# Optimization experiments

Hardware: AMD Instinct MI355X
Metric: run time of the kernel (lower is better)

The kernel has to match this reference:

```python
import jax, jax.numpy as jnp
import numpy as np

G = 7          # grid_size
A = 2          # anchors_per_cell
C = 3          # num_classes
L_COORD, L_OBJ, L_NOOBJ, L_CLS = 5.0, 1.0, 0.5, 2.0


def setup_inputs() -> dict:
    key = jax.random.key(0)
    k0, k1, k2, k3, k4 = jax.random.split(key, 5)
    B, M = 32768, 20
    predictions = jax.random.normal(k0, (B, G, G, A, 5 + C), dtype=jnp.float32)
    xy1 = jax.random.uniform(k1, (B, M, 2), dtype=jnp.float32) * 0.8
    wh = jax.random.uniform(k2, (B, M, 2), dtype=jnp.float32) * 0.19 + 0.01
    target_boxes = jnp.concatenate([xy1, xy1 + wh], axis=-1)  # valid x1<x2, y1<y2
    target_labels = jax.random.randint(k3, (B, M), 0, C, dtype=jnp.int32)
    num_objs = jax.random.randint(k4, (B,), 0, M + 1, dtype=jnp.int32)
    anchors = jnp.array([[0.971, 1.7338], [3.4579, 5.1653]], dtype=jnp.float32)
    class_weights = jnp.array([1.0, 4.9, 4.8], dtype=jnp.float32)
    return dict(predictions=predictions, target_boxes=target_boxes,
                target_labels=target_labels, num_objs=num_objs,
                anchors=anchors, class_weights=class_weights)


def assign_targets(target_boxes, target_labels, num_objs, anchors, B):
    """Vectorized scatter-based replacement of the nested python assignment loop."""
    M = target_boxes.shape[1]
    x1, y1, x2, y2 = [target_boxes[..., i] for i in range(4)]  # (B,M)
    cx, cy = (x1 + x2) * 0.5, (y1 + y2) * 0.5
    w, h = x2 - x1, y2 - y1
    valid = (w > 0) & (h > 0) & (jnp.arange(M)[None, :] < num_objs[:, None])
    gi = jnp.clip(jnp.floor(cy * G).astype(jnp.int32), 0, G - 1)
    gj = jnp.clip(jnp.floor(cx * G).astype(jnp.int32), 0, G - 1)
    wg, hg = w * G, h * G
    # anchor matching IoU (width/height only), (B,M,A)
    inter = jnp.minimum(wg[..., None], anchors[:, 0]) * jnp.minimum(hg[..., None], anchors[:, 1])
    union = (wg * hg)[..., None] + anchors[:, 0] * anchors[:, 1] - inter
    best_a = jnp.argmax(inter / (union + 1e-6), axis=-1).astype(jnp.int32)  # first max = torch loop tie-break
    aw = anchors[best_a, 0]
    ah = anchors[best_a, 1]
    tx = cx * G - gj.astype(jnp.float32)
    ty = cy * G - gi.astype(jnp.float32)
    tw = jnp.log(jnp.clip(wg, 0.01, None) / (aw + 1e-6))
    th = jnp.log(jnp.clip(hg, 0.01, None) / (ah + 1e-6))
    tvals = jnp.stack([tx, ty, tw, th], axis=-1)  # (B,M,4)
    N = B * G * G * A
    bidx = jnp.arange(B, dtype=jnp.int32)[:, None]
    flat = ((bidx * G + gi) * G + gj) * A + best_a  # (B,M)
    flat = jnp.where(valid, flat, N)                # invalid -> dropped by scatter
    idx = flat.ravel()
    obj_mask = jnp.zeros((N,), jnp.float32).at[idx].set(1.0, mode='drop')
    target_bbox = jnp.zeros((N, 4), jnp.float32).at[idx].set(tvals.reshape(-1, 4), mode='drop')
    target_cls = jnp.zeros((N,), jnp.int32).at[idx].set(target_labels.ravel(), mode='drop')
    shape = (B, G, G, A)
    return obj_mask.reshape(shape), target_bbox.reshape(shape + (4,)), target_cls.reshape(shape)


def reference(predictions, target_boxes, target_labels, num_objs, anchors, class_weights):
    B = predictions.shape[0]
    pred_obj = predictions[..., 0]
    pred_bbox = predictions[..., 1:5]
    pred_cls = predictions[..., 5:]
    m, target_bbox, target_cls = assign_targets(target_boxes, target_labels, num_objs, anchors, B)
    sp = jax.nn.softplus
    # BCE-with-logits: target is 1 on obj cells, 0 on noobj cells
    loss_obj = jnp.sum(m * sp(-pred_obj))
    loss_noobj = jnp.sum((1.0 - m) * sp(pred_obj))
    # smooth L1 (beta=1), summed over obj cells
    d = pred_bbox - target_bbox
    ad = jnp.abs(d)
    sl1 = jnp.where(ad < 1.0, 0.5 * d * d, ad - 0.5)
    loss_bbox = jnp.sum(m[..., None] * sl1)
    # weighted cross entropy on obj cells
    logZ = jax.nn.logsumexpimport if False else jax.scipy.special.logsumexp(pred_cls, axis=-1)
    logit_t = jnp.take_along_axis(pred_cls, target_cls[..., None], axis=-1)[..., 0]
    loss_cls = jnp.sum(m * class_weights[target_cls] * (logZ - logit_t))
    num_pos = jnp.maximum(jnp.sum(m), 1.0)
    total = (L_COORD * loss_bbox + L_OBJ * loss_obj + L_NOOBJ * loss_noobj + L_CLS * loss_cls) / num_pos
    return total
```

## Files before the change

### kernel.cpp

```cpp
#include <hip/hip_runtime.h>


namespace {
constexpr int kG = 7;
constexpr int kA = 2;
constexpr int kM = 20;
constexpr int kCells = kG * kG * kA;
constexpr int kCh = 8;
constexpr int kWavesA = 8;
constexpr int kBlockA = 64 * kWavesA;
constexpr int kBlockN = 256;
constexpr int kUnroll = 8;
constexpr int kChunksPerBlk = kBlockN * kUnroll;
}

typedef float f32x4 __attribute__((ext_vector_type(4)));

__device__ __forceinline__ float softplus_fast(float x) {
    return fmaxf(x, 0.0f) + __logf(1.0f + __expf(-fabsf(x)));
}

__global__ __launch_bounds__(kBlockA) void det_loss_assign(
    const float* __restrict__ preds,
    const float4* __restrict__ tboxes4,
    const int* __restrict__ tlabels,
    const int* __restrict__ nobjs,
    const float* __restrict__ anchors,
    const float* __restrict__ cweights,
    float* __restrict__ partialA,
    int B, int NA)
{
    __shared__ float s_red[kWavesA][5];

    const int tid  = threadIdx.x;
    const int wave = tid >> 6;
    const int m    = tid & 63;
    const int wb   = blockIdx.x * kWavesA + wave;
    const bool active = (wb < B);

    const float a00 = anchors[0], a01 = anchors[1];
    const float a10 = anchors[2], a11 = anchors[3];

    int nob = 0;
    if (active && m == 0) nob = nobjs[wb];
    nob = __shfl(nob, 0, 64);

    int cell = -1;
    float4 tv = make_float4(0.f, 0.f, 0.f, 0.f);
    if (active && m < kM) {
        const float4 box = tboxes4[(size_t)wb * kM + m];
        const float x1 = box.x, y1 = box.y, x2 = box.z, y2 = box.w;
        const float cx = (x1 + x2) * 0.5f, cy = (y1 + y2) * 0.5f;
        const float w = x2 - x1, h = y2 - y1;
        if (w > 0.f && h > 0.f && m < nob) {
            const int gi = min(max((int)floorf(cy * (float)kG), 0), kG - 1);
            const int gj = min(max((int)floorf(cx * (float)kG), 0), kG - 1);
            const float wg = w * (float)kG, hg = h * (float)kG;
            const float i0 = fminf(wg, a00) * fminf(hg, a01);
            const float u0 = wg * hg + a00 * a01 - i0;
            const float r0 = i0 / (u0 + 1e-6f);
            const float i1 = fminf(wg, a10) * fminf(hg, a11);
            const float u1 = wg * hg + a10 * a11 - i1;
            const float r1 = i1 / (u1 + 1e-6f);
            const int a = (r1 > r0) ? 1 : 0;
            const float aw = a ? a10 : a00;
            const float ah = a ? a11 : a01;
            tv.x = cx * (float)kG - (float)gj;
            tv.y = cy * (float)kG - (float)gi;
            tv.z = __logf(fmaxf(wg, 0.01f) / (aw + 1e-6f));
            tv.w = __logf(fmaxf(hg, 0.01f) / (ah + 1e-6f));
            cell = (gi * kG + gj) * kA + a;
        }
    }

    bool win = (cell >= 0);
    #pragma unroll
    for (int s = 1; s < kM; ++s) {
        const int other = __shfl_down(cell, s, 64);
        if ((m + s < kM) && (cell >= 0) && (other == cell)) win = false;
    }
    const unsigned long long bal = __ballot(win);

    float accO = 0.f, accN = 0.f, accB = 0.f, accC = 0.f;
    if (win) {
        const float4* pc = (const float4*)(preds + ((size_t)wb * kCells + cell) * kCh);
        const float4 p0 = pc[0];
        const float4 p1 = pc[1];
        const float spp = softplus_fast(p0.x);
        accN -= spp;
        accO += spp - p0.x;
        float d, ad;
        d = p0.y - tv.x; ad = fabsf(d); accB += (ad < 1.f) ? 0.5f * d * d : ad - 0.5f;
        d = p0.z - tv.y; ad = fabsf(d); accB += (ad < 1.f) ? 0.5f * d * d : ad - 0.5f;
        d = p0.w - tv.z; ad = fabsf(d); accB += (ad < 1.f) ? 0.5f * d * d : ad - 0.5f;
        d = p1.x - tv.w; ad = fabsf(d); accB += (ad < 1.f) ? 0.5f * d * d : ad - 0.5f;
        const int lab = tlabels[(size_t)wb * kM + m];
        const float c0 = p1.y, c1 = p1.z, c2 = p1.w;
        const float mx = fmaxf(c0, fmaxf(c1, c2));
        const float lse = mx + __logf(__expf(c0 - mx) + __expf(c1 - mx) + __expf(c2 - mx));
        const float logit = (lab == 0) ? c0 : ((lab == 1) ? c1 : c2);
        accC += cweights[lab] * (lse - logit);
    }

    float vals[4] = {accO, accN, accB, accC};
    #pragma unroll
    for (int k = 0; k < 4; ++k) {
        float v = vals[k];
        #pragma unroll
        for (int off = 32; off > 0; off >>= 1) v += __shfl_down(v, off, 64);
        vals[k] = v;
    }
    if (m == 0) {
        #pragma unroll
        for (int k = 0; k < 4; ++k) s_red[wave][k] = vals[k];
        s_red[wave][4] = (float)__popcll(bal);
    }
    __syncthreads();

    if (tid == 0) {
        float t[5];
        #pragma unroll
        for (int k = 0; k < 5; ++k) {
            float s = 0.f;
            #pragma unroll
            for (int w = 0; w < kWavesA; ++w) s += s_red[w][k];
            t[k] = s;
        }
        #pragma unroll
        for (int k = 0; k < 5; ++k)
            partialA[(size_t)k * NA + blockIdx.x] = t[k];
    }
}

__global__ __launch_bounds__(kBlockN) void det_loss_noobj(
    const f32x4* __restrict__ preds4,
    float* __restrict__ partialN,
    long long n4)
{
    __shared__ float s_red[kBlockN / 64];
    const int tid = threadIdx.x;
    const long long base = (long long)blockIdx.x * kChunksPerBlk + tid;

    f32x4 v[kUnroll];
    #pragma unroll
    for (int k = 0; k < kUnroll; ++k) {
        const long long i = base + (long long)k * kBlockN;
        v[k] = (i < n4) ? preds4[i] : (f32x4){0.f, 0.f, 0.f, 0.f};
    }

    float acc = 0.f;
    if ((tid & 1) == 0) {
        #pragma unroll
        for (int k = 0; k < kUnroll; ++k) {
            const long long i = base + (long long)k * kBlockN;
            if (i < n4) acc += softplus_fast(v[k].x);
        }
    }

    #pragma unroll
    for (int off = 32; off > 0; off >>= 1) acc += __shfl_down(acc, off, 64);
    if ((tid & 63) == 0) s_red[tid >> 6] = acc;
    __syncthreads();
    if (tid == 0) {
        float t = 0.f;
        #pragma unroll
        for (int w = 0; w < kBlockN / 64; ++w) t += s_red[w];
        partialN[blockIdx.x] = t;
    }
}

__global__ __launch_bounds__(256) void det_loss_reduce(
    const float* __restrict__ partialA, int NA,
    const float* __restrict__ partialN, int NN,
    float* __restrict__ out)
{
    __shared__ float s_red[4][5];
    const int tid = threadIdx.x;
    float v[5] = {0.f, 0.f, 0.f, 0.f, 0.f};
    for (int i = tid; i < NA; i += 256) {
        #pragma unroll
        for (int k = 0; k < 5; ++k) v[k] += partialA[(size_t)k * NA + i];
    }
    for (int i = tid; i < NN; i += 256) v[1] += partialN[i];
    #pragma unroll
    for (int k = 0; k < 5; ++k) {
        float x = v[k];
        #pragma unroll
        for (int off = 32; off > 0; off >>= 1) x += __shfl_down(x, off, 64);
        v[k] = x;
    }
    const int wave = tid >> 6;
    const int lane = tid & 63;
    if (lane == 0) {
        #pragma unroll
        for (int k = 0; k < 5; ++k) s_red[wave][k] = v[k];
    }
    __syncthreads();
    if (tid == 0) {
        float t[5];
        #pragma unroll
        for (int k = 0; k < 5; ++k) {
            float s = 0.f;
            #pragma unroll
            for (int w = 0; w < 4; ++w) s += s_red[w][k];
            t[k] = s;
        }
        const float npv = fmaxf(t[4], 1.0f);
        out[0] = (5.0f * t[2] + 1.0f * t[0] + 0.5f * t[1] + 2.0f * t[3]) / npv;
    }
}

extern "C" void kernel_launch(void* const* d_in, const int* in_sizes, int n_in,
                              void* d_out, int out_size, void* d_ws, size_t ws_size,
                              hipStream_t stream) {
    const float* preds    = (const float*)d_in[0];
    const float* tboxes   = (const float*)d_in[1];
    const int*   tlabels  = (const int*)d_in[2];
    const int*   nobjs    = (const int*)d_in[3];
    const float* anchors  = (const float*)d_in[4];
    const float* cweights = (const float*)d_in[5];
    float* out = (float*)d_out;

    const int B = in_sizes[0] / (kCells * kCh);
    const int blocksA = (B + kWavesA - 1) / kWavesA;
    const long long n4 = (long long)B * kCells * 2;
    const int blocksN = (int)((n4 + kChunksPerBlk - 1) / kChunksPerBlk);

    float* partialA = (float*)d_ws;
    float* partialN = partialA + (size_t)5 * blocksA;

    det_loss_assign<<<blocksA, kBlockA, 0, stream>>>(
        preds, (const float4*)tboxes, tlabels, nobjs, anchors, cweights,
        partialA, B, blocksA);
    det_loss_noobj<<<blocksN, kBlockN, 0, stream>>>(
        (const f32x4*)preds, partialN, n4);
    det_loss_reduce<<<1, 256, 0, stream>>>(partialA, blocksA, partialN, blocksN, out);
}
```

Baseline: 187.9 us.

## Stream noobj predictions through LDS with double-buffered direct global-to-LDS loads

Result: no change. 190.2 us (+1.3%).

```diff
diff --git a/kernel.cpp b/kernel.cpp
--- a/kernel.cpp
+++ b/kernel.cpp
@@ -10,11 +10,10 @@
 constexpr int kWavesA = 8;
 constexpr int kBlockA = 64 * kWavesA;
 constexpr int kBlockN = 256;
-constexpr int kUnroll = 8;
-constexpr int kChunksPerBlk = kBlockN * kUnroll;
-}
-
-typedef float f32x4 __attribute__((ext_vector_type(4)));
+constexpr int kWinChunks = 1024;
+constexpr int kNW = 4;
+constexpr int kChunksPerBlkN = kWinChunks * kNW;
+}
 
 __device__ __forceinline__ float softplus_fast(float x) {
     return fmaxf(x, 0.0f) + __logf(1.0f + __expf(-fabsf(x)));
@@ -133,33 +132,50 @@
 }
 
 __global__ __launch_bounds__(kBlockN) void det_loss_noobj(
-    const f32x4* __restrict__ preds4,
-    float* __restrict__ partialN,
-    long long n4)
+    const float4* __restrict__ preds4,
+    float* __restrict__ partialN)
 {
+    __shared__ float4 sbuf[2][kWinChunks];
     __shared__ float s_red[kBlockN / 64];
     const int tid = threadIdx.x;
-    const long long base = (long long)blockIdx.x * kChunksPerBlk + tid;
-
-    f32x4 v[kUnroll];
-    #pragma unroll
-    for (int k = 0; k < kUnroll; ++k) {
-        const long long i = base + (long long)k * kBlockN;
-        v[k] = (i < n4) ? preds4[i] : (f32x4){0.f, 0.f, 0.f, 0.f};
-    }
+    const int wv  = tid >> 6;
+    const int ln  = tid & 63;
+    const long long g0 = (long long)blockIdx.x * kChunksPerBlkN;
+
+    #define STAGE(DB, W)                                                        \
+        {                                                                       \
+            const long long base_ = g0 + (long long)(W) * kWinChunks + wv * 256 + ln; \
+            _Pragma("unroll")                                                   \
+            for (int c_ = 0; c_ < 4; ++c_) {                                    \
+                __builtin_amdgcn_global_load_lds(                               \
+                    (const __attribute__((address_space(1))) void*)(preds4 + base_ + c_ * 64), \
+                    (__attribute__((address_space(3))) void*)&sbuf[(DB)][wv * 256 + c_ * 64], \
+                    16, 0, 0);                                                  \
+            }                                                                   \
+        }
 
     float acc = 0.f;
-    if ((tid & 1) == 0) {
-        #pragma unroll
-        for (int k = 0; k < kUnroll; ++k) {
-            const long long i = base + (long long)k * kBlockN;
-            if (i < n4) acc += softplus_fast(v[k].x);
-        }
-    }
+    STAGE(0, 0)
+    #pragma unroll
+    for (int w = 0; w < kNW; ++w) {
+        const int db = w & 1;
+        if (w + 1 < kNW) {
+            STAGE((w + 1) & 1, w + 1)
+            asm volatile("s_waitcnt vmcnt(4)" ::: "memory");
+        } else {
+            asm volatile("s_waitcnt vmcnt(0)" ::: "memory");
+        }
+        __builtin_amdgcn_sched_barrier(0);
+        const float o0 = sbuf[db][wv * 256 + 2 * ln].x;
+        const float o1 = sbuf[db][wv * 256 + 2 * ln + 128].x;
+        acc += softplus_fast(o0) + softplus_fast(o1);
+        __builtin_amdgcn_sched_barrier(0);
+    }
+    #undef STAGE
 
     #pragma unroll
     for (int off = 32; off > 0; off >>= 1) acc += __shfl_down(acc, off, 64);
-    if ((tid & 63) == 0) s_red[tid >> 6] = acc;
+    if (ln == 0) s_red[wv] = acc;
     __syncthreads();
     if (tid == 0) {
         float t = 0.f;
@@ -172,6 +188,7 @@
 __global__ __launch_bounds__(256) void det_loss_reduce(
     const float* __restrict__ partialA, int NA,
     const float* __restrict__ partialN, int NN,
+    const float4* __restrict__ preds4, long long remStart, long long n4,
     float* __restrict__ out)
 {
     __shared__ float s_red[4][5];
@@ -182,6 +199,8 @@
         for (int k = 0; k < 5; ++k) v[k] += partialA[(size_t)k * NA + i];
     }
     for (int i = tid; i < NN; i += 256) v[1] += partialN[i];
+    for (long long i = remStart + 2 * tid; i < n4; i += 512)
+        v[1] += softplus_fast(preds4[i].x);
     #pragma unroll
     for (int k = 0; k < 5; ++k) {
         float x = v[k];
@@ -224,7 +243,8 @@
     const int B = in_sizes[0] / (kCells * kCh);
     const int blocksA = (B + kWavesA - 1) / kWavesA;
     const long long n4 = (long long)B * kCells * 2;
-    const int blocksN = (int)((n4 + kChunksPerBlk - 1) / kChunksPerBlk);
+    const int blocksN = (int)(n4 / kChunksPerBlkN);
+    const long long remStart = (long long)blocksN * kChunksPerBlkN;
 
     float* partialA = (float*)d_ws;
     float* partialN = partialA + (size_t)5 * blocksA;
@@ -232,7 +252,10 @@
     det_loss_assign<<<blocksA, kBlockA, 0, stream>>>(
         preds, (const float4*)tboxes, tlabels, nobjs, anchors, cweights,
         partialA, B, blocksA);
-    det_loss_noobj<<<blocksN, kBlockN, 0, stream>>>(
-        (const f32x4*)preds, partialN, n4);
-    det_loss_reduce<<<1, 256, 0, stream>>>(partialA, blocksA, partialN, blocksN, out);
-}
+    if (blocksN > 0)
+        det_loss_noobj<<<blocksN, kBlockN, 0, stream>>>(
+            (const float4*)preds, partialN);
+    det_loss_reduce<<<1, 256, 0, stream>>>(
+        partialA, blocksA, partialN, blocksN,
+        (const float4*)preds, remStart, n4, out);
+}
```
